# Performance work log

Measured on AMD Instinct MI355X. Metric: run time of the kernel, lower is better.

## Reference

```python
import jax, jax.numpy as jnp
import numpy as np

N_NODES = 40000
N_EDGES = 640000
D_IN = 128
D_OUT = 128
LN_EPS = 1e-5


def setup_inputs() -> dict:
    key = jax.random.key(0)
    ks = jax.random.split(key, 8)
    x = jax.random.normal(ks[0], (N_NODES, D_IN), dtype=jnp.float32)
    edge_index = jax.random.randint(ks[1], (2, N_EDGES), 0, N_NODES, dtype=jnp.int64)
    edge_weight_mean = jax.random.normal(ks[2], (N_EDGES,), dtype=jnp.float32)
    edge_weight_var = jax.random.uniform(ks[3], (N_EDGES,), dtype=jnp.float32)
    s = 1.0 / np.sqrt(D_IN)
    W_mean = jax.random.normal(ks[4], (D_IN, D_OUT), dtype=jnp.float32) * s
    b_mean = jax.random.normal(ks[5], (D_OUT,), dtype=jnp.float32) * 0.01
    W_logvar = jax.random.normal(ks[6], (D_IN, D_OUT), dtype=jnp.float32) * s
    b_logvar = jax.random.normal(ks[7], (D_OUT,), dtype=jnp.float32) * 0.01
    gamma = jnp.ones((D_OUT,), dtype=jnp.float32)
    beta = jnp.zeros((D_OUT,), dtype=jnp.float32)
    return {"x": x, "edge_index": edge_index, "edge_weight_mean": edge_weight_mean,
            "edge_weight_var": edge_weight_var, "W_mean": W_mean, "b_mean": b_mean,
            "W_logvar": W_logvar, "b_logvar": b_logvar, "gamma": gamma, "beta": beta}


def reference(x, edge_index, edge_weight_mean, edge_weight_var,
              W_mean, b_mean, W_logvar, b_logvar, gamma, beta):
    num_nodes = x.shape[0]
    h_mean = x @ W_mean + b_mean                      # [N, C]
    h_var = jnp.exp(x @ W_logvar + b_logvar)          # [N, C]
    row, col = edge_index[0], edge_index[1]
    ewm = edge_weight_mean[:, None]                   # [E, 1]
    ewv = edge_weight_var[:, None]                    # [E, 1]
    hm_c = h_mean[col]                                # gather [E, C]
    hv_c = h_var[col]
    msg_mean = hm_c * ewm
    msg_var = ewm ** 2 * hv_c + hm_c ** 2 * ewv
    out_mean = jax.ops.segment_sum(msg_mean, row, num_segments=num_nodes)
    out_var = jax.ops.segment_sum(msg_var, row, num_segments=num_nodes)
    degree = jax.ops.segment_sum(jnp.ones_like(edge_weight_mean), row, num_segments=num_nodes)
    degree = jnp.clip(degree, 1.0)[:, None]
    out_mean = out_mean / degree
    out_var = out_var / degree ** 2
    # LayerNorm over last dim (dropout is identity in eval mode)
    mu = jnp.mean(out_mean, axis=-1, keepdims=True)
    var = jnp.mean((out_mean - mu) ** 2, axis=-1, keepdims=True)
    out_mean = (out_mean - mu) * jax.lax.rsqrt(var + LN_EPS) * gamma + beta
    return (out_mean, out_var)
```

## Files before the change

### kernel.cpp

```cpp
#include <hip/hip_runtime.h>
#include <hip/hip_bf16.h>
#include <math.h>

#define N_NODES 40000
#define N_EDGES 640000
#define D 128
#define LN_EPS 1e-5f
#define STRIDE 48

typedef __attribute__((ext_vector_type(8))) short bf16x8;
typedef __attribute__((ext_vector_type(4))) float f32x4;

__device__ __forceinline__ unsigned bf2pack(float a, float b) {
    unsigned ua = __float_as_uint(a);
    ua = (ua + 0x7fffu + ((ua >> 16) & 1u)) >> 16;
    unsigned ub = __float_as_uint(b);
    ub = (ub + 0x7fffu + ((ub >> 16) & 1u)) >> 16;
    return ua | (ub << 16);
}
__device__ __forceinline__ unsigned short bfr(float a) {
    unsigned ua = __float_as_uint(a);
    return (unsigned short)((ua + 0x7fffu + ((ua >> 16) & 1u)) >> 16);
}
__device__ __forceinline__ float bflo(unsigned u) { return __uint_as_float(u << 16); }
__device__ __forceinline__ float bfhi(unsigned u) { return __uint_as_float(u & 0xffff0000u); }

__global__ __launch_bounds__(256) void packw_kernel(
    const float* __restrict__ Wm, const float* __restrict__ Wv,
    const float* __restrict__ bm, const float* __restrict__ bv,
    unsigned short* __restrict__ Wpk, float* __restrict__ bcat,
    int* __restrict__ counts)
{
    int idx = blockIdx.x * 256 + threadIdx.x;
    if (idx < N_NODES) counts[idx] = 0;
    if (idx < 256) bcat[idx] = (idx < 128) ? bm[idx] : bv[idx - 128];
    if (idx >= 32768) return;
    int j  = idx & 7;
    int l  = (idx >> 3) & 63;
    int nt = (idx >> 9) & 15;
    int kt = idx >> 13;
    int k = kt * 32 + (l >> 4) * 8 + j;
    int c = nt * 16 + (l & 15);
    float w = (c < 128) ? Wm[k * 128 + c] : Wv[k * 128 + (c - 128)];
    Wpk[idx] = bfr(w);
}

__global__ __launch_bounds__(256) void gemm_kernel(
    const float* __restrict__ x, const unsigned short* __restrict__ Wpk,
    const float* __restrict__ bcat, unsigned* __restrict__ hb,
    const int* __restrict__ row, const int* __restrict__ col,
    const float* __restrict__ ewm, const float* __restrict__ ewv,
    int* __restrict__ counts, float4* __restrict__ epack)
{
    const int gid = blockIdx.x * 256 + threadIdx.x;
    int2 r = ((const int2*)row)[gid];
    int k0 = atomicAdd(&counts[r.x], 1);
    int k1 = atomicAdd(&counts[r.y], 1);

    {
        const int w = threadIdx.x >> 6;
        const int l = threadIdx.x & 63;
        const int rbase = blockIdx.x * 32 + (w & 1) * 16;
        const int colh = w >> 1;
        const int arow = rbase + (l & 15);
        const int kqo = (l >> 4) * 8;

        bf16x8 a[4];
        #pragma unroll
        for (int kt = 0; kt < 4; ++kt) {
            const float* ap = &x[(size_t)arow * 128 + kt * 32 + kqo];
            float4 lo = *(const float4*)ap;
            float4 hi = *(const float4*)(ap + 4);
            uint4 au;
            au.x = bf2pack(lo.x, lo.y); au.y = bf2pack(lo.z, lo.w);
            au.z = bf2pack(hi.x, hi.y); au.w = bf2pack(hi.z, hi.w);
            a[kt] = *(bf16x8*)&au;
        }

        f32x4 accm[4], accv[4];
        #pragma unroll
        for (int i = 0; i < 4; ++i) {
            accm[i] = (f32x4){0.f, 0.f, 0.f, 0.f};
            accv[i] = (f32x4){0.f, 0.f, 0.f, 0.f};
        }

        const bf16x8* wp = (const bf16x8*)Wpk;
        #pragma unroll
        for (int kt = 0; kt < 4; ++kt) {
            #pragma unroll
            for (int i = 0; i < 4; ++i) {
                int ntm = colh * 4 + i;
                int ntv = 8 + colh * 4 + i;
                bf16x8 bmf = wp[(kt * 16 + ntm) * 64 + l];
                bf16x8 bvf = wp[(kt * 16 + ntv) * 64 + l];
                accm[i] = __builtin_amdgcn_mfma_f32_16x16x32_bf16(a[kt], bmf, accm[i], 0, 0, 0);
                accv[i] = __builtin_amdgcn_mfma_f32_16x16x32_bf16(a[kt], bvf, accv[i], 0, 0, 0);
            }
        }

        const int c0 = l & 15;
        const int rq = rbase + (l >> 4) * 4;
        #pragma unroll
        for (int i = 0; i < 4; ++i) {
            int feat = colh * 64 + i * 16 + c0;
            float bmv = bcat[feat];
            float bvv = bcat[128 + feat];
            #pragma unroll
            for (int q = 0; q < 4; ++q) {
                float m = accm[i][q] + bmv;
                float v = expf(accv[i][q] + bvv);
                hb[(size_t)(rq + q) * 128 + feat] = bf2pack(m, v);
            }
        }
    }

    {
        int2   c2 = ((const int2*)col)[gid];
        float2 wm = ((const float2*)ewm)[gid];
        float2 wv = ((const float2*)ewv)[gid];
        if (k0 < STRIDE) epack[(size_t)r.x * STRIDE + k0] =
            make_float4(__int_as_float(c2.x), wm.x, wv.x, 0.0f);
        if (k1 < STRIDE) epack[(size_t)r.y * STRIDE + k1] =
            make_float4(__int_as_float(c2.y), wm.y, wv.y, 0.0f);
    }
}

__device__ __forceinline__ void accum_edge(
    const uint4& h, float wm, float wv, float (&am)[4], float (&av)[4])
{
    float wm2 = wm * wm;
    float mf, vf;
    mf = bflo(h.x); vf = bfhi(h.x);
    am[0] = fmaf(mf, wm, am[0]);
    av[0] = fmaf(wm2, vf, fmaf(mf * mf, wv, av[0]));
    mf = bflo(h.y); vf = bfhi(h.y);
    am[1] = fmaf(mf, wm, am[1]);
    av[1] = fmaf(wm2, vf, fmaf(mf * mf, wv, av[1]));
    mf = bflo(h.z); vf = bfhi(h.z);
    am[2] = fmaf(mf, wm, am[2]);
    av[2] = fmaf(wm2, vf, fmaf(mf * mf, wv, av[2]));
    mf = bflo(h.w); vf = bfhi(h.w);
    am[3] = fmaf(mf, wm, am[3]);
    av[3] = fmaf(wm2, vf, fmaf(mf * mf, wv, av[3]));
}

__global__ __launch_bounds__(256) void agg_kernel(
    const uint4* __restrict__ hb, const int* __restrict__ counts,
    const float4* __restrict__ epack,
    const float* __restrict__ gamma, const float* __restrict__ beta,
    float* __restrict__ out)
{
    const int wid  = threadIdx.x >> 6;
    const int lane = threadIdx.x & 63;
    const int half = lane >> 5;
    const int sub  = lane & 31;
    const int n = blockIdx.x * 4 + wid;

    const int start = n * STRIDE;
    int cnt = counts[n];
    cnt = cnt < STRIDE ? cnt : STRIDE;
    const int end = start + cnt;

    float am[4] = {}, av[4] = {};

    int e = start;
    for (; e + 8 <= end; e += 8) {
        float4 m[4]; uint4 h[4];
        #pragma unroll
        for (int i = 0; i < 4; ++i) m[i] = epack[e + 2 * i + half];
        #pragma unroll
        for (int i = 0; i < 4; ++i) {
            int c = __float_as_int(m[i].x);
            h[i] = hb[(size_t)c * 32 + sub];
        }
        #pragma unroll
        for (int i = 0; i < 4; ++i) accum_edge(h[i], m[i].y, m[i].z, am, av);
    }
    for (; e + 2 <= end; e += 2) {
        float4 m = epack[e + half];
        int c = __float_as_int(m.x);
        uint4 h = hb[(size_t)c * 32 + sub];
        accum_edge(h, m.y, m.z, am, av);
    }
    if (e < end && half == 0) {
        float4 m = epack[e];
        int c = __float_as_int(m.x);
        uint4 h = hb[(size_t)c * 32 + sub];
        accum_edge(h, m.y, m.z, am, av);
    }

    #pragma unroll
    for (int j = 0; j < 4; ++j) {
        am[j] += __shfl_xor(am[j], 32);
        av[j] += __shfl_xor(av[j], 32);
    }

    float degi = 1.0f / fmaxf((float)cnt, 1.0f);
    float dg2 = degi * degi;
    #pragma unroll
    for (int j = 0; j < 4; ++j) { am[j] *= degi; av[j] *= dg2; }

    float s = am[0] + am[1] + am[2] + am[3];
    #pragma unroll
    for (int off = 16; off >= 1; off >>= 1) s += __shfl_xor(s, off);
    float mu = s * (1.0f / 128.0f);
    float d0 = am[0] - mu, d1 = am[1] - mu, d2 = am[2] - mu, d3 = am[3] - mu;
    float q = d0 * d0 + d1 * d1 + d2 * d2 + d3 * d3;
    #pragma unroll
    for (int off = 16; off >= 1; off >>= 1) q += __shfl_xor(q, off);
    float var = q * (1.0f / 128.0f);
    float rs = rsqrtf(var + LN_EPS);

    if (half == 0) {
        float4 g = *(const float4*)&gamma[sub * 4];
        float4 b = *(const float4*)&beta[sub * 4];
        float4 om = make_float4(fmaf(d0 * rs, g.x, b.x), fmaf(d1 * rs, g.y, b.y),
                                fmaf(d2 * rs, g.z, b.z), fmaf(d3 * rs, g.w, b.w));
        *(float4*)&out[(size_t)n * D + sub * 4] = om;
        *(float4*)&out[(size_t)N_NODES * D + (size_t)n * D + sub * 4] =
            make_float4(av[0], av[1], av[2], av[3]);
    }
}

extern "C" void kernel_launch(void* const* d_in, const int* in_sizes, int n_in,
                              void* d_out, int out_size, void* d_ws, size_t ws_size,
                              hipStream_t stream)
{
    const float* x     = (const float*)d_in[0];
    const int*   eidx  = (const int*)d_in[1];
    const float* ewm   = (const float*)d_in[2];
    const float* ewv   = (const float*)d_in[3];
    const float* Wm    = (const float*)d_in[4];
    const float* bm    = (const float*)d_in[5];
    const float* Wv    = (const float*)d_in[6];
    const float* bv    = (const float*)d_in[7];
    const float* gamma = (const float*)d_in[8];
    const float* beta  = (const float*)d_in[9];
    const int* row = eidx;
    const int* col = eidx + N_EDGES;

    char* ws = (char*)d_ws;
    size_t off = 0;
    auto alloc = [&](size_t bytes) {
        void* p = ws + off;
        off += (bytes + 255) & ~(size_t)255;
        return p;
    };
    unsigned* hb        = (unsigned*)alloc((size_t)N_NODES * 512);
    unsigned short* Wpk = (unsigned short*)alloc(32768 * 2);
    float* bcat    = (float*)alloc(256 * 4);
    int*   counts  = (int*)alloc((size_t)N_NODES * 4);
    float4* epack  = (float4*)alloc((size_t)N_NODES * STRIDE * 16);

    packw_kernel<<<160, 256, 0, stream>>>(Wm, Wv, bm, bv, Wpk, bcat, counts);
    gemm_kernel<<<1250, 256, 0, stream>>>(
        x, Wpk, bcat, hb, row, col, ewm, ewv, counts, epack);
    agg_kernel<<<N_NODES / 4, 256, 0, stream>>>(
        (const uint4*)hb, counts, epack, gamma, beta, (float*)d_out);
}
```

Baseline: 93.22 us.

## Split edge histogram/scatter out of GEMM kernel and widen GEMM tiles per wave

The edge counting and scatter into per-node buckets is moved out of the GEMM kernel into a separate one-edge-per-thread kernel. The GEMM now has each wave compute all 16 output tiles (mean and logvar) for 16 rows, 64 rows per block. This separates the atomic-heavy scatter from the MFMA work, so each kernel can use its own launch shape and the GEMM reuses its A fragments across all N tiles. The cost is an extra kernel launch, the loss of overlap between the two phases inside one kernel, and 64 accumulator vector registers per thread, which may lower occupancy.

```diff
diff --git a/kernel.cpp b/kernel.cpp
--- a/kernel.cpp
+++ b/kernel.cpp
@@ -47,82 +47,68 @@
 
 __global__ __launch_bounds__(256) void gemm_kernel(
     const float* __restrict__ x, const unsigned short* __restrict__ Wpk,
-    const float* __restrict__ bcat, unsigned* __restrict__ hb,
+    const float* __restrict__ bcat, unsigned* __restrict__ hb)
+{
+    const int w = threadIdx.x >> 6;
+    const int l = threadIdx.x & 63;
+    const int rbase = blockIdx.x * 64 + w * 16;
+    const int arow = rbase + (l & 15);
+    const int kqo = (l >> 4) * 8;
+
+    bf16x8 a[4];
+    #pragma unroll
+    for (int kt = 0; kt < 4; ++kt) {
+        const float* ap = &x[(size_t)arow * 128 + kt * 32 + kqo];
+        float4 lo = *(const float4*)ap;
+        float4 hi = *(const float4*)(ap + 4);
+        uint4 au;
+        au.x = bf2pack(lo.x, lo.y); au.y = bf2pack(lo.z, lo.w);
+        au.z = bf2pack(hi.x, hi.y); au.w = bf2pack(hi.z, hi.w);
+        a[kt] = *(bf16x8*)&au;
+    }
+
+    f32x4 acc[16];
+    #pragma unroll
+    for (int nt = 0; nt < 16; ++nt) acc[nt] = (f32x4){0.f, 0.f, 0.f, 0.f};
+
+    const bf16x8* wp = (const bf16x8*)Wpk;
+    #pragma unroll
+    for (int kt = 0; kt < 4; ++kt) {
+        #pragma unroll
+        for (int nt = 0; nt < 16; ++nt) {
+            bf16x8 b = wp[(kt * 16 + nt) * 64 + l];
+            acc[nt] = __builtin_amdgcn_mfma_f32_16x16x32_bf16(a[kt], b, acc[nt], 0, 0, 0);
+        }
+    }
+
+    const int c0 = l & 15;
+    const int rq = rbase + (l >> 4) * 4;
+    #pragma unroll
+    for (int nt = 0; nt < 8; ++nt) {
+        float bmv = bcat[nt * 16 + c0];
+        float bvv = bcat[128 + nt * 16 + c0];
+        #pragma unroll
+        for (int q = 0; q < 4; ++q) {
+            float m = acc[nt][q] + bmv;
+            float v = expf(acc[nt + 8][q] + bvv);
+            hb[(size_t)(rq + q) * 128 + nt * 16 + c0] = bf2pack(m, v);
+        }
+    }
+}
+
+__global__ __launch_bounds__(256) void hist_scatter_kernel(
     const int* __restrict__ row, const int* __restrict__ col,
     const float* __restrict__ ewm, const float* __restrict__ ewv,
     int* __restrict__ counts, float4* __restrict__ epack)
 {
-    const int gid = blockIdx.x * 256 + threadIdx.x;
-    int2 r = ((const int2*)row)[gid];
-    int k0 = atomicAdd(&counts[r.x], 1);
-    int k1 = atomicAdd(&counts[r.y], 1);
-
-    {
-        const int w = threadIdx.x >> 6;
-        const int l = threadIdx.x & 63;
-        const int rbase = blockIdx.x * 32 + (w & 1) * 16;
-        const int colh = w >> 1;
-        const int arow = rbase + (l & 15);
-        const int kqo = (l >> 4) * 8;
-
-        bf16x8 a[4];
-        #pragma unroll
-        for (int kt = 0; kt < 4; ++kt) {
-            const float* ap = &x[(size_t)arow * 128 + kt * 32 + kqo];
-            float4 lo = *(const float4*)ap;
-            float4 hi = *(const float4*)(ap + 4);
-            uint4 au;
-            au.x = bf2pack(lo.x, lo.y); au.y = bf2pack(lo.z, lo.w);
-            au.z = bf2pack(hi.x, hi.y); au.w = bf2pack(hi.z, hi.w);
-            a[kt] = *(bf16x8*)&au;
-        }
-
-        f32x4 accm[4], accv[4];
-        #pragma unroll
-        for (int i = 0; i < 4; ++i) {
-            accm[i] = (f32x4){0.f, 0.f, 0.f, 0.f};
-            accv[i] = (f32x4){0.f, 0.f, 0.f, 0.f};
-        }
-
-        const bf16x8* wp = (const bf16x8*)Wpk;
-        #pragma unroll
-        for (int kt = 0; kt < 4; ++kt) {
-            #pragma unroll
-            for (int i = 0; i < 4; ++i) {
-                int ntm = colh * 4 + i;
-                int ntv = 8 + colh * 4 + i;
-                bf16x8 bmf = wp[(kt * 16 + ntm) * 64 + l];
-                bf16x8 bvf = wp[(kt * 16 + ntv) * 64 + l];
-                accm[i] = __builtin_amdgcn_mfma_f32_16x16x32_bf16(a[kt], bmf, accm[i], 0, 0, 0);
-                accv[i] = __builtin_amdgcn_mfma_f32_16x16x32_bf16(a[kt], bvf, accv[i], 0, 0, 0);
-            }
-        }
-
-        const int c0 = l & 15;
-        const int rq = rbase + (l >> 4) * 4;
-        #pragma unroll
-        for (int i = 0; i < 4; ++i) {
-            int feat = colh * 64 + i * 16 + c0;
-            float bmv = bcat[feat];
-            float bvv = bcat[128 + feat];
-            #pragma unroll
-            for (int q = 0; q < 4; ++q) {
-                float m = accm[i][q] + bmv;
-                float v = expf(accv[i][q] + bvv);
-                hb[(size_t)(rq + q) * 128 + feat] = bf2pack(m, v);
-            }
-        }
-    }
-
-    {
-        int2   c2 = ((const int2*)col)[gid];
-        float2 wm = ((const float2*)ewm)[gid];
-        float2 wv = ((const float2*)ewv)[gid];
-        if (k0 < STRIDE) epack[(size_t)r.x * STRIDE + k0] =
-            make_float4(__int_as_float(c2.x), wm.x, wv.x, 0.0f);
-        if (k1 < STRIDE) epack[(size_t)r.y * STRIDE + k1] =
-            make_float4(__int_as_float(c2.y), wm.y, wv.y, 0.0f);
-    }
+    int e = blockIdx.x * 256 + threadIdx.x;
+    int r = row[e];
+    int c = col[e];
+    float wm = ewm[e], wv = ewv[e];
+    int k = atomicAdd(&counts[r], 1);
+    if (k < STRIDE)
+        epack[(size_t)r * STRIDE + k] =
+            make_float4(__int_as_float(c), wm, wv, 0.0f);
 }
 
 __device__ __forceinline__ void accum_edge(
@@ -253,8 +239,9 @@
     float4* epack  = (float4*)alloc((size_t)N_NODES * STRIDE * 16);
 
     packw_kernel<<<160, 256, 0, stream>>>(Wm, Wv, bm, bv, Wpk, bcat, counts);
-    gemm_kernel<<<1250, 256, 0, stream>>>(
-        x, Wpk, bcat, hb, row, col, ewm, ewv, counts, epack);
+    gemm_kernel<<<N_NODES / 64, 256, 0, stream>>>(x, Wpk, bcat, hb);
+    hist_scatter_kernel<<<N_EDGES / 256, 256, 0, stream>>>(
+        row, col, ewm, ewv, counts, epack);
     agg_kernel<<<N_NODES / 4, 256, 0, stream>>>(
         (const uint4*)hb, counts, epack, gamma, beta, (float*)d_out);
 }
```

Result: slower. 105.3 us (+12.9%).
